# Optimization experiments

Measured on AMD Instinct MI355X. Metric: run time of the kernel, lower is better.

The kernel has to match this reference:

```python
import jax, jax.numpy as jnp
import numpy as np

B_, S, D = 4, 1024, 1024
MULT, HEAD_DIM, M, K, CFAC = 4, 64, 16, 2, 1.25
H = MULT * D


def _layer_norm(x, g, b, eps=1e-5):
    mu = jnp.mean(x, axis=-1, keepdims=True)
    var = jnp.var(x, axis=-1, keepdims=True)
    return (x - mu) * jax.lax.rsqrt(var + eps) * g + b


def setup_inputs() -> dict:
    key = jax.random.key(0)
    ks = jax.random.split(key, 10)
    sc = 0.02
    return {
        "x": jax.random.normal(ks[0], (B_, S, D), jnp.float32),
        "ln1_g": jnp.ones((D,), jnp.float32), "ln1_b": jnp.zeros((D,), jnp.float32),
        "qkv_w": jax.random.normal(ks[1], (3 * D, D), jnp.float32) * sc,
        "qkv_b": jnp.zeros((3 * D,), jnp.float32),
        "attn_in_w": jax.random.normal(ks[2], (3 * D, D), jnp.float32) * sc,
        "attn_in_b": jnp.zeros((3 * D,), jnp.float32),
        "attn_out_w": jax.random.normal(ks[3], (D, D), jnp.float32) * sc,
        "attn_out_b": jnp.zeros((D,), jnp.float32),
        "ln2_g": jnp.ones((D,), jnp.float32), "ln2_b": jnp.zeros((D,), jnp.float32),
        "r_w1": jax.random.normal(ks[4], (H, D), jnp.float32) * sc,
        "r_b1": jnp.zeros((H,), jnp.float32),
        "r_w2": jax.random.normal(ks[5], (M, H), jnp.float32) * sc,
        "r_b2": jnp.zeros((M,), jnp.float32),
        "mlp1": jax.random.normal(ks[6], (M, D, H), jnp.float32) / np.float32(np.sqrt(D)),
        "mlp2": jax.random.normal(ks[7], (M, H, D), jnp.float32) / np.float32(np.sqrt(H)),
    }


def reference(x, ln1_g, ln1_b, qkv_w, qkv_b, attn_in_w, attn_in_b,
              attn_out_w, attn_out_b, ln2_g, ln2_b, r_w1, r_b1, r_w2, r_b2,
              mlp1, mlp2):
    b, s, d = x.shape
    nh, hd = d // HEAD_DIM, HEAD_DIM

    # ---- attention block ----
    resid = x
    xn = _layer_norm(x, ln1_g, ln1_b)
    qkv = xn @ qkv_w.T + qkv_b              # [b,s,3d]
    q0, k0, v0 = jnp.split(qkv, 3, axis=-1)
    # nn.MultiheadAttention applies its own in/out projections on top
    wq, wk, wv = jnp.split(attn_in_w, 3, axis=0)
    bq, bk, bv = jnp.split(attn_in_b, 3, axis=0)
    q = (q0 @ wq.T + bq).reshape(b, s, nh, hd).transpose(0, 2, 1, 3)
    k = (k0 @ wk.T + bk).reshape(b, s, nh, hd).transpose(0, 2, 1, 3)
    v = (v0 @ wv.T + bv).reshape(b, s, nh, hd).transpose(0, 2, 1, 3)
    scores = jnp.einsum('bhqd,bhkd->bhqk', q, k) / np.float32(np.sqrt(hd))
    causal = jnp.triu(jnp.full((s, s), -jnp.inf, jnp.float32), k=1)
    attn = jax.nn.softmax(scores + causal, axis=-1)
    ao = jnp.einsum('bhqk,bhkd->bhqd', attn, v).transpose(0, 2, 1, 3).reshape(b, s, d)
    x1 = resid + (ao @ attn_out_w.T + attn_out_b)

    # ---- MoE MLP block ----
    resid2 = x1
    xn2 = _layer_norm(x1, ln2_g, ln2_b)
    B = b * s
    cap = int(B * CFAC * K // M)
    xf = xn2.reshape(B, d)
    # router
    logits = jax.nn.gelu(xf @ r_w1.T + r_b1, approximate=False) @ r_w2.T + r_b2  # [B,M]
    vals, inds = jax.lax.top_k(logits, K)
    probs = jax.nn.softmax(vals, axis=-1).reshape(-1)     # [B*K]
    indsf = inds.reshape(-1)                              # [B*K]
    # cumsum-based position within each expert's capacity buffer
    one_hot = jax.nn.one_hot(indsf, M, dtype=jnp.int32)
    counts = jnp.cumsum(one_hot, axis=0)
    pos = counts[jnp.arange(B * K), indsf] - 1
    keep = pos < cap
    flat_idx = indsf * cap + pos
    safe_idx = jnp.where(keep, flat_idx, M * cap)         # OOB index -> dropped
    src = jnp.repeat(xf, K, axis=0)                       # [B*K, d]
    expert_in = jnp.zeros((M * cap, d), xf.dtype).at[safe_idx].set(src, mode='drop')
    expert_in = expert_in.reshape(M, cap, d)
    # grouped GEMM experts
    mid = jax.nn.gelu(jnp.einsum('mcd,mdh->mch', expert_in, mlp1), approximate=False)
    eout = jnp.einsum('mch,mhd->mcd', mid, mlp2).reshape(M * cap, d)
    # combine
    g = eout[jnp.where(keep, flat_idx, 0)] * (probs * keep)[:, None]
    token_idx = jnp.repeat(jnp.arange(B), K)
    combined = jax.ops.segment_sum(g, token_idx, num_segments=B)
    has_kept = jax.ops.segment_sum(keep.astype(jnp.int32), token_idx, num_segments=B) > 0
    moe_out = jnp.where(has_kept[:, None], combined, xf)
    out = resid2 + moe_out.reshape(b, s, d)
    return out, logits.reshape(b, s, M)
```

## Files before the change

kernel.cpp:

```cpp
#include <hip/hip_runtime.h>
#include <math.h>

#define NTOK   4096
#define DIM    1024
#define H3     3072
#define HMLP   4096
#define NEXP   16
#define CAP    640
#define HCHUNK 1024
#define LSCALE 2048.0f
#define INV_LSCALE (1.0f / 2048.0f)

typedef _Float16 half8 __attribute__((ext_vector_type(8)));
typedef __attribute__((ext_vector_type(4))) float floatx4;
typedef __attribute__((ext_vector_type(8))) ushort us8;

#define F_QKV_HI   ((size_t)0)
#define F_QKV_LO   ((size_t)6291456)
#define F_XN_HI    ((size_t)12582912)
#define F_XN_LO    ((size_t)14680064)
#define F_H1       ((size_t)0)
#define F_EOUT     ((size_t)0)
#define F_Q16_HI   ((size_t)16777216)
#define F_K16_HI   ((size_t)18874368)
#define F_V16_HI   ((size_t)20971520)
#define F_Q16_LO   ((size_t)23068672)
#define F_K16_LO   ((size_t)25165824)
#define F_V16_LO   ((size_t)27262976)
#define F_VT_HI    ((size_t)12582912)
#define F_VT_LO    ((size_t)14680064)
#define F_AO_HI    ((size_t)29360128)
#define F_AO_LO    ((size_t)31457280)
#define F_XF_HI    ((size_t)33554432)
#define F_XF_LO    ((size_t)35651584)
#define F_WQKV_HI  ((size_t)37748736)
#define F_WQKV_LO  ((size_t)39321600)
#define F_WAIN_HI  ((size_t)40894464)
#define F_WAIN_LO  ((size_t)42467328)
#define F_WAOUT_HI ((size_t)44040192)
#define F_WAOUT_LO ((size_t)44564480)
#define F_WR1_HI   ((size_t)45088768)
#define F_WR1_LO   ((size_t)47185920)
#define F_EXPIN    ((size_t)16777216)
#define F_MLP1T    ((size_t)22020096)
#define F_MID      ((size_t)30408704)
#define F_MLP2T    ((size_t)35651584)
#define F_X1       ((size_t)49283072)
#define F_XF       ((size_t)53477376)
#define F_PROBS    ((size_t)57671680)
#define F_INDS     ((size_t)57679872)
#define F_KEEP     ((size_t)57688064)
#define F_FLAT     ((size_t)57696256)

__device__ __forceinline__ ushort f2h(float f) {
    _Float16 h = (_Float16)f;
    union { _Float16 h; ushort u; } c; c.h = h; return c.u;
}
__device__ __forceinline__ float h2f(ushort u) {
    union { ushort u; _Float16 h; } c; c.u = u; return (float)c.h;
}
__device__ __forceinline__ float gelu_exact(float x) {
    return 0.5f * x * (1.0f + erff(x * 0.7071067811865475f));
}

__global__ __launch_bounds__(256) void split_f32(const float* __restrict__ x,
                                                 ushort* __restrict__ hi,
                                                 ushort* __restrict__ lo, int n4) {
    int i = blockIdx.x * 256 + threadIdx.x;
    if (i >= n4) return;
    float4 v = ((const float4*)x)[i];
    float vv[4] = {v.x, v.y, v.z, v.w};
    ushort h[4], l[4];
#pragma unroll
    for (int e = 0; e < 4; e++) {
        h[e] = f2h(vv[e]);
        l[e] = f2h((vv[e] - h2f(h[e])) * LSCALE);
    }
    ((ushort4*)hi)[i] = make_ushort4(h[0], h[1], h[2], h[3]);
    ((ushort4*)lo)[i] = make_ushort4(l[0], l[1], l[2], l[3]);
}

__global__ __launch_bounds__(256) void ln_kernel(const float* __restrict__ x,
                                                 const float* __restrict__ g,
                                                 const float* __restrict__ b,
                                                 float* __restrict__ yf,
                                                 ushort* __restrict__ yhi,
                                                 ushort* __restrict__ ylo) {
    __shared__ float red0[4], red1[4], bc[2];
    const size_t t = blockIdx.x;
    const float* row = x + t * DIM;
    float v[4];
    float s = 0.f, s2 = 0.f;
#pragma unroll
    for (int i = 0; i < 4; i++) {
        float vv = row[threadIdx.x + i * 256];
        v[i] = vv; s += vv; s2 += vv * vv;
    }
#pragma unroll
    for (int off = 32; off > 0; off >>= 1) {
        s  += __shfl_down(s, off);
        s2 += __shfl_down(s2, off);
    }
    const int lane = threadIdx.x & 63, wid = threadIdx.x >> 6;
    if (lane == 0) { red0[wid] = s; red1[wid] = s2; }
    __syncthreads();
    if (threadIdx.x == 0) {
        float S = red0[0] + red0[1] + red0[2] + red0[3];
        float S2 = red1[0] + red1[1] + red1[2] + red1[3];
        float mean = S * (1.0f / DIM);
        float var = S2 * (1.0f / DIM) - mean * mean;
        bc[0] = mean; bc[1] = rsqrtf(var + 1e-5f);
    }
    __syncthreads();
    const float mean = bc[0], r = bc[1];
#pragma unroll
    for (int i = 0; i < 4; i++) {
        int idx = threadIdx.x + i * 256;
        float val = (v[i] - mean) * r * g[idx] + b[idx];
        size_t o = t * DIM + idx;
        if (yf) yf[o] = val;
        if (yhi) {
            ushort h = f2h(val);
            yhi[o] = h;
            if (ylo) ylo[o] = f2h((val - h2f(h)) * LSCALE);
        }
    }
}

template<bool SPLIT>
__global__ __launch_bounds__(256) void gemm_ht(
    const ushort* __restrict__ Ahi, const ushort* __restrict__ Alo, int lda, long long sA,
    const ushort* __restrict__ Bhi, const ushort* __restrict__ Blo, int ldb, long long sB,
    const float* __restrict__ bias, long long sBias,
    const float* __restrict__ resid, int ldr,
    float* __restrict__ outf, ushort* __restrict__ outhi, ushort* __restrict__ outlo,
    int ldc, long long sC, int Kdim, int act, int accum) {
    __shared__ ushort sAh[128][40];
    __shared__ ushort sBh[128][40];
    __shared__ ushort sAl[SPLIT ? 128 : 1][40];
    __shared__ ushort sBl[SPLIT ? 128 : 1][40];
    const int z = blockIdx.z;
    Ahi += (size_t)z * sA; Bhi += (size_t)z * sB;
    if constexpr (SPLIT) { Alo += (size_t)z * sA; Blo += (size_t)z * sB; }
    if (bias) bias += (size_t)z * sBias;
    if (outf) outf += (size_t)z * sC;
    if (outhi) outhi += (size_t)z * sC;
    if (outlo) outlo += (size_t)z * sC;

    const int tid = threadIdx.x;
    const int row0 = blockIdx.y * 128, col0 = blockIdx.x * 128;
    const int sr = tid >> 2, skq = (tid & 3) * 8;
    const int lane = tid & 63;
    const int m = lane & 15, half = lane >> 4;
    const int w = tid >> 6;
    const int ar0 = (w >> 1) * 64, bc0 = (w & 1) * 64;

    floatx4 acc[4][4];
    floatx4 acc2[SPLIT ? 4 : 1][SPLIT ? 4 : 1];
#pragma unroll
    for (int i = 0; i < 4; i++)
#pragma unroll
        for (int j = 0; j < 4; j++) acc[i][j] = (floatx4){0.f, 0.f, 0.f, 0.f};
    if constexpr (SPLIT) {
#pragma unroll
        for (int i = 0; i < 4; i++)
#pragma unroll
            for (int j = 0; j < 4; j++) acc2[i][j] = (floatx4){0.f, 0.f, 0.f, 0.f};
    }

    for (int k0 = 0; k0 < Kdim; k0 += 32) {
        uint4 a0 = *(const uint4*)(Ahi + (size_t)(row0 + sr) * lda + k0 + skq);
        uint4 a1 = *(const uint4*)(Ahi + (size_t)(row0 + sr + 64) * lda + k0 + skq);
        uint4 b0 = *(const uint4*)(Bhi + (size_t)(col0 + sr) * ldb + k0 + skq);
        uint4 b1 = *(const uint4*)(Bhi + (size_t)(col0 + sr + 64) * ldb + k0 + skq);
        uint4 a2, a3, b2, b3;
        if constexpr (SPLIT) {
            a2 = *(const uint4*)(Alo + (size_t)(row0 + sr) * lda + k0 + skq);
            a3 = *(const uint4*)(Alo + (size_t)(row0 + sr + 64) * lda + k0 + skq);
            b2 = *(const uint4*)(Blo + (size_t)(col0 + sr) * ldb + k0 + skq);
            b3 = *(const uint4*)(Blo + (size_t)(col0 + sr + 64) * ldb + k0 + skq);
        }
        __syncthreads();
        *(uint4*)&sAh[sr][skq] = a0;
        *(uint4*)&sAh[sr + 64][skq] = a1;
        *(uint4*)&sBh[sr][skq] = b0;
        *(uint4*)&sBh[sr + 64][skq] = b1;
        if constexpr (SPLIT) {
            *(uint4*)&sAl[sr][skq] = a2;
            *(uint4*)&sAl[sr + 64][skq] = a3;
            *(uint4*)&sBl[sr][skq] = b2;
            *(uint4*)&sBl[sr + 64][skq] = b3;
        }
        __syncthreads();
        half8 fa[4], fb[4], fal[4], fbl[4];
#pragma unroll
        for (int i = 0; i < 4; i++) fa[i] = *(const half8*)&sAh[ar0 + i * 16 + m][half * 8];
#pragma unroll
        for (int j = 0; j < 4; j++) fb[j] = *(const half8*)&sBh[bc0 + j * 16 + m][half * 8];
        if constexpr (SPLIT) {
#pragma unroll
            for (int i = 0; i < 4; i++) fal[i] = *(const half8*)&sAl[ar0 + i * 16 + m][half * 8];
#pragma unroll
            for (int j = 0; j < 4; j++) fbl[j] = *(const half8*)&sBl[bc0 + j * 16 + m][half * 8];
        }
#pragma unroll
        for (int i = 0; i < 4; i++)
#pragma unroll
            for (int j = 0; j < 4; j++) {
                acc[i][j] = __builtin_amdgcn_mfma_f32_16x16x32_f16(fa[i], fb[j], acc[i][j], 0, 0, 0);
                if constexpr (SPLIT) {
                    acc2[i][j] = __builtin_amdgcn_mfma_f32_16x16x32_f16(fa[i], fbl[j], acc2[i][j], 0, 0, 0);
                    acc2[i][j] = __builtin_amdgcn_mfma_f32_16x16x32_f16(fal[i], fb[j], acc2[i][j], 0, 0, 0);
                }
            }
    }
#pragma unroll
    for (int i = 0; i < 4; i++) {
#pragma unroll
        for (int j = 0; j < 4; j++) {
            const int col = col0 + bc0 + j * 16 + m;
            const float bv = bias ? bias[col] : 0.f;
#pragma unroll
            for (int r = 0; r < 4; r++) {
                const int row = row0 + ar0 + i * 16 + half * 4 + r;
                float v = acc[i][j][r];
                if constexpr (SPLIT) v += acc2[i][j][r] * INV_LSCALE;
                v += bv;
                if (resid) v += resid[(size_t)row * ldr + col];
                if (accum) v += outf[(size_t)row * ldc + col];
                if (act) v = gelu_exact(v);
                const size_t o = (size_t)row * ldc + col;
                if (outf) outf[o] = v;
                if (outhi) {
                    ushort h = f2h(v);
                    outhi[o] = h;
                    if (outlo) outlo[o] = f2h((v - h2f(h)) * LSCALE);
                }
            }
        }
    }
}

__global__ __launch_bounds__(256) void transpose_h(const float* __restrict__ in, long long sIn, int ldin,
                                                   ushort* __restrict__ out, long long sOut, int ldout) {
    __shared__ float t[32][33];
    const int z = blockIdx.z;
    in += (size_t)z * sIn; out += (size_t)z * sOut;
    const int cx = threadIdx.x & 31, ry = threadIdx.x >> 5;
    const int r0 = blockIdx.y * 32, c0 = blockIdx.x * 32;
#pragma unroll
    for (int rr = 0; rr < 4; rr++)
        t[ry + rr * 8][cx] = in[(size_t)(r0 + ry + rr * 8) * ldin + c0 + cx];
    __syncthreads();
#pragma unroll
    for (int rr = 0; rr < 4; rr++)
        out[(size_t)(c0 + ry + rr * 8) * ldout + r0 + cx] = f2h(t[cx][ry + rr * 8]);
}

__global__ __launch_bounds__(256) void vtrans_kernel(const ushort* __restrict__ vhi,
                                                     const ushort* __restrict__ vlo,
                                                     ushort* __restrict__ vthi,
                                                     ushort* __restrict__ vtlo) {
    __shared__ ushort th[32][72], tl[32][72];
    const int bh = blockIdx.y, b = bh >> 4, h = bh & 15;
    const int s0 = blockIdx.x * 32;
    const int t = threadIdx.x;
    {
        const int s = t >> 3, d0 = (t & 7) * 8;
        const size_t src = ((size_t)(b * 1024 + s0 + s)) * 1024 + h * 64 + d0;
        *(uint4*)&th[s][d0] = *(const uint4*)&vhi[src];
        *(uint4*)&tl[s][d0] = *(const uint4*)&vlo[src];
    }
    __syncthreads();
    {
        const int d = t >> 2, soff = (t & 3) * 8;
        us8 rh, rl;
#pragma unroll
        for (int e = 0; e < 8; e++) { rh[e] = th[soff + e][d]; rl[e] = tl[soff + e][d]; }
        const size_t dst = (size_t)bh * 65536 + (size_t)d * 1024 + s0 + soff;
        *(us8*)&vthi[dst] = rh;
        *(us8*)&vtlo[dst] = rl;
    }
}

__global__ __launch_bounds__(256, 2) void attn_mfma(
        const ushort* __restrict__ qh_, const ushort* __restrict__ ql_,
        const ushort* __restrict__ kh_, const ushort* __restrict__ kl_,
        const ushort* __restrict__ vth_, const ushort* __restrict__ vtl_,
        ushort* __restrict__ ao_hi, ushort* __restrict__ ao_lo) {
    __shared__ ushort plds[4][2][2048];
    const int bh = blockIdx.y;
    const int b = bh >> 4;
    const int qt = 7 - blockIdx.x;
    const int tid = threadIdx.x;
    const int w = tid >> 6, lane = tid & 63;
    const int m = lane & 15, hq = lane >> 4;
    const int wrow = qt * 128 + w * 32;
    const size_t cbase = ((size_t)b * 1024) * 1024 + (size_t)(bh & 15) * 64;
    const size_t vtbase = (size_t)bh * 65536;

    half8 qfh[2][2], qfl[2][2];
#pragma unroll
    for (int i = 0; i < 2; i++)
#pragma unroll
        for (int kk = 0; kk < 2; kk++) {
            const size_t o = cbase + (size_t)(wrow + i * 16 + m) * 1024 + kk * 32 + hq * 8;
            qfh[i][kk] = *(const half8*)&qh_[o];
            qfl[i][kk] = *(const half8*)&ql_[o];
        }

    floatx4 accO[2][4], accO2[2][4];
#pragma unroll
    for (int i = 0; i < 2; i++)
#pragma unroll
        for (int d = 0; d < 4; d++) {
            accO[i][d] = (floatx4){0.f, 0.f, 0.f, 0.f};
            accO2[i][d] = (floatx4){0.f, 0.f, 0.f, 0.f};
        }
    float mx[2][4], ls[2][4];
#pragma unroll
    for (int i = 0; i < 2; i++)
#pragma unroll
        for (int r = 0; r < 4; r++) { mx[i][r] = -3.0e38f; ls[i][r] = 0.f; }

    const int ntiles = (wrow + 31) / 64 + 1;
    for (int t = 0; t < ntiles; t++) {
        const int j0 = t * 64;
        floatx4 accS[2][4], accS2[2][4];
#pragma unroll
        for (int i = 0; i < 2; i++)
#pragma unroll
            for (int jf = 0; jf < 4; jf++) {
                accS[i][jf] = (floatx4){0.f, 0.f, 0.f, 0.f};
                accS2[i][jf] = (floatx4){0.f, 0.f, 0.f, 0.f};
            }
#pragma unroll
        for (int kk = 0; kk < 2; kk++) {
            half8 kfh[4], kfl[4];
#pragma unroll
            for (int jf = 0; jf < 4; jf++) {
                const size_t o = cbase + (size_t)(j0 + jf * 16 + m) * 1024 + kk * 32 + hq * 8;
                kfh[jf] = *(const half8*)&kh_[o];
                kfl[jf] = *(const half8*)&kl_[o];
            }
#pragma unroll
            for (int i = 0; i < 2; i++)
#pragma unroll
                for (int jf = 0; jf < 4; jf++) {
                    accS[i][jf] = __builtin_amdgcn_mfma_f32_16x16x32_f16(qfh[i][kk], kfh[jf], accS[i][jf], 0, 0, 0);
                    accS2[i][jf] = __builtin_amdgcn_mfma_f32_16x16x32_f16(qfh[i][kk], kfl[jf], accS2[i][jf], 0, 0, 0);
                    accS2[i][jf] = __builtin_amdgcn_mfma_f32_16x16x32_f16(qfl[i][kk], kfh[jf], accS2[i][jf], 0, 0, 0);
                }
        }
        const bool diag = (j0 + 63 > wrow);
        float p[2][4][4];
#pragma unroll
        for (int i = 0; i < 2; i++)
#pragma unroll
            for (int jf = 0; jf < 4; jf++)
#pragma unroll
                for (int r = 0; r < 4; r++) {
                    float s = (accS[i][jf][r] + accS2[i][jf][r] * INV_LSCALE) * 0.125f;
                    if (diag && (j0 + jf * 16 + m > wrow + i * 16 + hq * 4 + r)) s = -3.0e38f;
                    p[i][jf][r] = s;
                }
#pragma unroll
        for (int i = 0; i < 2; i++)
#pragma unroll
            for (int r = 0; r < 4; r++) {
                float tm = fmaxf(fmaxf(p[i][0][r], p[i][1][r]), fmaxf(p[i][2][r], p[i][3][r]));
#pragma unroll
                for (int off = 8; off > 0; off >>= 1) tm = fmaxf(tm, __shfl_xor(tm, off));
                const float mn = fmaxf(mx[i][r], tm);
                const float c = __expf(mx[i][r] - mn);
                mx[i][r] = mn;
                float rs = 0.f;
#pragma unroll
                for (int jf = 0; jf < 4; jf++) {
                    const float e = __expf(p[i][jf][r] - mn);
                    p[i][jf][r] = e;
                    rs += e;
                }
#pragma unroll
                for (int off = 8; off > 0; off >>= 1) rs += __shfl_xor(rs, off);
                ls[i][r] = ls[i][r] * c + rs;
#pragma unroll
                for (int d = 0; d < 4; d++) { accO[i][d][r] *= c; accO2[i][d][r] *= c; }
            }
#pragma unroll
        for (int i = 0; i < 2; i++)
#pragma unroll
            for (int jf = 0; jf < 4; jf++)
#pragma unroll
                for (int r = 0; r < 4; r++) {
                    const int row = i * 16 + hq * 4 + r;
                    const int idx = row * 64 + ((jf * 16 + m) ^ ((row & 7) << 3));
                    const float pv = p[i][jf][r];
                    const ushort hh = f2h(pv);
                    plds[w][0][idx] = hh;
                    plds[w][1][idx] = f2h((pv - h2f(hh)) * LSCALE);
                }
#pragma unroll
        for (int kk = 0; kk < 2; kk++) {
            half8 pfh[2], pfl[2], vfh[4], vfl[4];
#pragma unroll
            for (int i = 0; i < 2; i++) {
                const int row = i * 16 + m;
                const int idx = row * 64 + ((kk * 32 + hq * 8) ^ ((row & 7) << 3));
                pfh[i] = *(const half8*)&plds[w][0][idx];
                pfl[i] = *(const half8*)&plds[w][1][idx];
            }
#pragma unroll
            for (int d = 0; d < 4; d++) {
                const size_t o = vtbase + (size_t)(d * 16 + m) * 1024 + j0 + kk * 32 + hq * 8;
                vfh[d] = *(const half8*)&vth_[o];
                vfl[d] = *(const half8*)&vtl_[o];
            }
#pragma unroll
            for (int i = 0; i < 2; i++)
#pragma unroll
                for (int d = 0; d < 4; d++) {
                    accO[i][d] = __builtin_amdgcn_mfma_f32_16x16x32_f16(pfh[i], vfh[d], accO[i][d], 0, 0, 0);
                    accO2[i][d] = __builtin_amdgcn_mfma_f32_16x16x32_f16(pfh[i], vfl[d], accO2[i][d], 0, 0, 0);
                    accO2[i][d] = __builtin_amdgcn_mfma_f32_16x16x32_f16(pfl[i], vfh[d], accO2[i][d], 0, 0, 0);
                }
        }
    }
#pragma unroll
    for (int i = 0; i < 2; i++)
#pragma unroll
        for (int r = 0; r < 4; r++) {
            const float inv = 1.f / ls[i][r];
            const size_t rb = cbase + (size_t)(wrow + i * 16 + hq * 4 + r) * 1024;
#pragma unroll
            for (int d = 0; d < 4; d++) {
                const float v = (accO[i][d][r] + accO2[i][d][r] * INV_LSCALE) * inv;
                const ushort hh = f2h(v);
                const size_t o = rb + d * 16 + m;
                ao_hi[o] = hh;
                ao_lo[o] = f2h((v - h2f(hh)) * LSCALE);
            }
        }
}

__global__ __launch_bounds__(256) void router2_kernel(const float* __restrict__ h1,
                                                      const float* __restrict__ w2,
                                                      const float* __restrict__ b2,
                                                      float* __restrict__ logits_out,
                                                      float* __restrict__ probs,
                                                      int* __restrict__ inds) {
    __shared__ float red[16][4];
    __shared__ float lg[16];
    const int t = blockIdx.x;
    const float* hrow = h1 + (size_t)t * HMLP;
    float acc[16];
#pragma unroll
    for (int m = 0; m < 16; m++) acc[m] = 0.f;
    for (int i = 0; i < 16; i++) {
        int kk = threadIdx.x + i * 256;
        float hv = hrow[kk];
#pragma unroll
        for (int m = 0; m < 16; m++) acc[m] = fmaf(hv, w2[m * HMLP + kk], acc[m]);
    }
#pragma unroll
    for (int m = 0; m < 16; m++)
#pragma unroll
        for (int off = 32; off > 0; off >>= 1) acc[m] += __shfl_down(acc[m], off);
    const int lane = threadIdx.x & 63, wid = threadIdx.x >> 6;
    if (lane == 0) {
#pragma unroll
        for (int m = 0; m < 16; m++) red[m][wid] = acc[m];
    }
    __syncthreads();
    if (threadIdx.x < 16) {
        float v = red[threadIdx.x][0] + red[threadIdx.x][1] + red[threadIdx.x][2] + red[threadIdx.x][3]
                  + b2[threadIdx.x];
        lg[threadIdx.x] = v;
        logits_out[(size_t)t * 16 + threadIdx.x] = v;
    }
    __syncthreads();
    if (threadIdx.x == 0) {
        int i0 = 0; float v0 = lg[0];
        for (int m = 1; m < 16; m++) if (lg[m] > v0) { v0 = lg[m]; i0 = m; }
        int i1 = -1; float v1 = -3.4e38f;
        for (int m = 0; m < 16; m++) if (m != i0 && lg[m] > v1) { v1 = lg[m]; i1 = m; }
        float e1 = expf(v1 - v0);
        float den = 1.f + e1;
        inds[2 * t] = i0; inds[2 * t + 1] = i1;
        probs[2 * t] = 1.f / den; probs[2 * t + 1] = e1 / den;
    }
}

__global__ __launch_bounds__(256) void scan_kernel(const int* __restrict__ inds,
                                                   int* __restrict__ keep,
                                                   int* __restrict__ flat) {
    __shared__ int counts[256][16];
    const int t = threadIdx.x;
#pragma unroll
    for (int e = 0; e < 16; e++) counts[t][e] = 0;
    const int base = t * 32;
    for (int i = 0; i < 32; i++) counts[t][inds[base + i]]++;
    __syncthreads();
    if (t < 16) {
        int run = 0;
        for (int c = 0; c < 256; c++) { int tmp = counts[c][t]; counts[c][t] = run; run += tmp; }
    }
    __syncthreads();
    for (int i = 0; i < 32; i++) {
        int e = inds[base + i];
        int p = counts[t][e]++;
        keep[base + i] = (p < CAP) ? 1 : 0;
        flat[base + i] = e * CAP + p;
    }
}

__global__ __launch_bounds__(256) void scatter_kernel(const float* __restrict__ xf,
                                                      const int* __restrict__ keep,
                                                      const int* __restrict__ flat,
                                                      ushort* __restrict__ expert_in) {
    const int e = blockIdx.x;
    if (!keep[e]) return;
    const int token = e >> 1;
    const float* src = xf + (size_t)token * DIM;
    ushort* dst = expert_in + (size_t)flat[e] * DIM;
#pragma unroll
    for (int i = 0; i < 4; i++) dst[threadIdx.x + i * 256] = f2h(src[threadIdx.x + i * 256]);
}

__global__ __launch_bounds__(256) void combine_kernel(const float* __restrict__ x1,
                                                      const float* __restrict__ xf,
                                                      const float* __restrict__ eout,
                                                      const float* __restrict__ probs,
                                                      const int* __restrict__ keep,
                                                      const int* __restrict__ flat,
                                                      float* __restrict__ out) {
    const int t = blockIdx.x;
    const int k0 = keep[2 * t], k1 = keep[2 * t + 1];
    const float p0 = probs[2 * t], p1 = probs[2 * t + 1];
    const size_t f0 = (size_t)flat[2 * t] * DIM, f1 = (size_t)flat[2 * t + 1] * DIM;
    const bool has = (k0 || k1);
    const size_t base = (size_t)t * DIM;
#pragma unroll
    for (int i = 0; i < 4; i++) {
        const int idx = threadIdx.x + i * 256;
        float mo;
        if (has) {
            mo = 0.f;
            if (k0) mo += p0 * eout[f0 + idx];
            if (k1) mo += p1 * eout[f1 + idx];
        } else {
            mo = xf[base + idx];
        }
        out[base + idx] = x1[base + idx] + mo;
    }
}

extern "C" void kernel_launch(void* const* d_in, const int* in_sizes, int n_in,
                              void* d_out, int out_size, void* d_ws, size_t ws_size,
                              hipStream_t stream) {
    const float* x          = (const float*)d_in[0];
    const float* ln1_g      = (const float*)d_in[1];
    const float* ln1_b      = (const float*)d_in[2];
    const float* qkv_w      = (const float*)d_in[3];
    const float* qkv_b      = (const float*)d_in[4];
    const float* attn_in_w  = (const float*)d_in[5];
    const float* attn_in_b  = (const float*)d_in[6];
    const float* attn_out_w = (const float*)d_in[7];
    const float* attn_out_b = (const float*)d_in[8];
    const float* ln2_g      = (const float*)d_in[9];
    const float* ln2_b      = (const float*)d_in[10];
    const float* r_w1       = (const float*)d_in[11];
    const float* r_b1       = (const float*)d_in[12];
    const float* r_w2       = (const float*)d_in[13];
    const float* r_b2       = (const float*)d_in[14];
    const float* mlp1       = (const float*)d_in[15];
    const float* mlp2       = (const float*)d_in[16];

    float* ws = (float*)d_ws;
    ushort* qkv_hi   = (ushort*)(ws + F_QKV_HI);
    ushort* qkv_lo   = (ushort*)(ws + F_QKV_LO);
    ushort* xn_hi    = (ushort*)(ws + F_XN_HI);
    ushort* xn_lo    = (ushort*)(ws + F_XN_LO);
    float*  h1       = ws + F_H1;
    float*  eout     = ws + F_EOUT;
    ushort* q_hi     = (ushort*)(ws + F_Q16_HI);
    ushort* q_lo     = (ushort*)(ws + F_Q16_LO);
    ushort* v_hi     = (ushort*)(ws + F_V16_HI);
    ushort* v_lo     = (ushort*)(ws + F_V16_LO);
    ushort* k_hi     = (ushort*)(ws + F_K16_HI);
    ushort* k_lo     = (ushort*)(ws + F_K16_LO);
    ushort* vt_hi    = (ushort*)(ws + F_VT_HI);
    ushort* vt_lo    = (ushort*)(ws + F_VT_LO);
    ushort* ao_hi    = (ushort*)(ws + F_AO_HI);
    ushort* ao_lo    = (ushort*)(ws + F_AO_LO);
    ushort* xf_hi    = (ushort*)(ws + F_XF_HI);
    ushort* xf_lo    = (ushort*)(ws + F_XF_LO);
    ushort* wqkv_hi  = (ushort*)(ws + F_WQKV_HI);
    ushort* wqkv_lo  = (ushort*)(ws + F_WQKV_LO);
    ushort* wain_hi  = (ushort*)(ws + F_WAIN_HI);
    ushort* wain_lo  = (ushort*)(ws + F_WAIN_LO);
    ushort* waout_hi = (ushort*)(ws + F_WAOUT_HI);
    ushort* waout_lo = (ushort*)(ws + F_WAOUT_LO);
    ushort* wr1_hi   = (ushort*)(ws + F_WR1_HI);
    ushort* wr1_lo   = (ushort*)(ws + F_WR1_LO);
    ushort* expert_in= (ushort*)(ws + F_EXPIN);
    ushort* mlp1t    = (ushort*)(ws + F_MLP1T);
    ushort* mid      = (ushort*)(ws + F_MID);
    ushort* mlp2t    = (ushort*)(ws + F_MLP2T);
    float*  x1       = ws + F_X1;
    float*  xf       = ws + F_XF;
    float*  probs    = ws + F_PROBS;
    int*    inds     = (int*)(ws + F_INDS);
    int*    keep     = (int*)(ws + F_KEEP);
    int*    flat     = (int*)(ws + F_FLAT);

    float* out        = (float*)d_out;
    float* logits_out = out + (size_t)NTOK * DIM;

    split_f32<<<(3145728 / 4 + 255) / 256, 256, 0, stream>>>(qkv_w, wqkv_hi, wqkv_lo, 3145728 / 4);
    split_f32<<<(3145728 / 4 + 255) / 256, 256, 0, stream>>>(attn_in_w, wain_hi, wain_lo, 3145728 / 4);
    split_f32<<<(1048576 / 4 + 255) / 256, 256, 0, stream>>>(attn_out_w, waout_hi, waout_lo, 1048576 / 4);
    split_f32<<<(4194304 / 4 + 255) / 256, 256, 0, stream>>>(r_w1, wr1_hi, wr1_lo, 4194304 / 4);

    ln_kernel<<<NTOK, 256, 0, stream>>>(x, ln1_g, ln1_b, nullptr, xn_hi, xn_lo);
    gemm_ht<true><<<dim3(H3 / 128, NTOK / 128, 1), 256, 0, stream>>>(
        xn_hi, xn_lo, DIM, 0, wqkv_hi, wqkv_lo, DIM, 0, qkv_b, 0,
        nullptr, 0, nullptr, qkv_hi, qkv_lo, H3, 0, DIM, 0, 0);
    gemm_ht<true><<<dim3(DIM / 128, NTOK / 128, 3), 256, 0, stream>>>(
        qkv_hi, qkv_lo, H3, 1024, wain_hi, wain_lo, DIM, 1048576, attn_in_b, 1024,
        nullptr, 0, nullptr, q_hi, q_lo, DIM, 4194304, DIM, 0, 0);
    vtrans_kernel<<<dim3(32, 64), 256, 0, stream>>>(v_hi, v_lo, vt_hi, vt_lo);
    attn_mfma<<<dim3(8, 64), 256, 0, stream>>>(q_hi, q_lo, k_hi, k_lo, vt_hi, vt_lo, ao_hi, ao_lo);
    gemm_ht<true><<<dim3(DIM / 128, NTOK / 128, 1), 256, 0, stream>>>(
        ao_hi, ao_lo, DIM, 0, waout_hi, waout_lo, DIM, 0, attn_out_b, 0,
        x, DIM, x1, nullptr, nullptr, DIM, 0, DIM, 0, 0);
    ln_kernel<<<NTOK, 256, 0, stream>>>(x1, ln2_g, ln2_b, xf, xf_hi, xf_lo);
    gemm_ht<true><<<dim3(HMLP / 128, NTOK / 128, 1), 256, 0, stream>>>(
        xf_hi, xf_lo, DIM, 0, wr1_hi, wr1_lo, DIM, 0, r_b1, 0,
        nullptr, 0, h1, nullptr, nullptr, HMLP, 0, DIM, 1, 0);
    router2_kernel<<<NTOK, 256, 0, stream>>>(h1, r_w2, r_b2, logits_out, probs, inds);
    scan_kernel<<<1, 256, 0, stream>>>(inds, keep, flat);
    scatter_kernel<<<NTOK * 2, 256, 0, stream>>>(xf, keep, flat, expert_in);
    for (int c = 0; c < HMLP / HCHUNK; c++) {
        transpose_h<<<dim3(32, 32, NEXP), 256, 0, stream>>>(
            mlp1 + (size_t)c * HCHUNK, (long long)DIM * HMLP, HMLP, mlp1t, 1048576, DIM);
        gemm_ht<false><<<dim3(HCHUNK / 128, CAP / 128, NEXP), 256, 0, stream>>>(
            expert_in, nullptr, DIM, 655360, mlp1t, nullptr, DIM, 1048576, nullptr, 0,
            nullptr, 0, nullptr, mid, nullptr, HCHUNK, 655360, DIM, 1, 0);
        transpose_h<<<dim3(32, 32, NEXP), 256, 0, stream>>>(
            mlp2 + (size_t)c * HCHUNK * DIM, (long long)HMLP * DIM, DIM, mlp2t, 1048576, HCHUNK);
        gemm_ht<false><<<dim3(DIM / 128, CAP / 128, NEXP), 256, 0, stream>>>(
            mid, nullptr, HCHUNK, 655360, mlp2t, nullptr, HCHUNK, 1048576, nullptr, 0,
            nullptr, 0, eout, nullptr, nullptr, DIM, 655360, HCHUNK, 0, c > 0);
    }
    combine_kernel<<<NTOK, 256, 0, stream>>>(x1, xf, eout, probs, keep, flat, out);
}
```

Baseline: 2.315 ms.

## Load GEMM tiles directly into LDS with global_load_lds and XOR swizzle

Replaces the register-staged global→LDS tile copies in the half-precision GEMM with direct global_load_lds 16-byte transfers. The padded LDS rows (40) become unpadded (32), and an XOR swizzle on both the write column and the fragment read column is meant to avoid bank conflicts. This cuts VGPR use and copy instructions, but the loads are still issued right after a barrier with no double buffering, so the latency is not hidden. It also depends on the swizzle mapping matching between writer and reader.

```diff
diff --git a/kernel.cpp b/kernel.cpp
--- a/kernel.cpp
+++ b/kernel.cpp
@@ -63,6 +63,12 @@
     return 0.5f * x * (1.0f + erff(x * 0.7071067811865475f));
 }
 
+__device__ __forceinline__ void gl16(const void* g, void* l) {
+    __builtin_amdgcn_global_load_lds(
+        (const __attribute__((address_space(1))) void*)g,
+        (__attribute__((address_space(3))) void*)l, 16, 0, 0);
+}
+
 __global__ __launch_bounds__(256) void split_f32(const float* __restrict__ x,
                                                  ushort* __restrict__ hi,
                                                  ushort* __restrict__ lo, int n4) {
@@ -135,10 +141,10 @@
     const float* __restrict__ resid, int ldr,
     float* __restrict__ outf, ushort* __restrict__ outhi, ushort* __restrict__ outlo,
     int ldc, long long sC, int Kdim, int act, int accum) {
-    __shared__ ushort sAh[128][40];
-    __shared__ ushort sBh[128][40];
-    __shared__ ushort sAl[SPLIT ? 128 : 1][40];
-    __shared__ ushort sBl[SPLIT ? 128 : 1][40];
+    __shared__ ushort sAh[128][32];
+    __shared__ ushort sBh[128][32];
+    __shared__ ushort sAl[SPLIT ? 128 : 1][32];
+    __shared__ ushort sBl[SPLIT ? 128 : 1][32];
     const int z = blockIdx.z;
     Ahi += (size_t)z * sA; Bhi += (size_t)z * sB;
     if constexpr (SPLIT) { Alo += (size_t)z * sA; Blo += (size_t)z * sB; }
@@ -149,12 +155,15 @@
 
     const int tid = threadIdx.x;
     const int row0 = blockIdx.y * 128, col0 = blockIdx.x * 128;
-    const int sr = tid >> 2, skq = (tid & 3) * 8;
     const int lane = tid & 63;
     const int m = lane & 15, half = lane >> 4;
     const int w = tid >> 6;
     const int ar0 = (w >> 1) * 64, bc0 = (w & 1) * 64;
 
+    const int srow = w * 32 + (lane >> 2);
+    const int ssw  = (((lane >> 3) & 3) ^ (lane & 3)) * 8;
+    const int rsw8 = ((((m >> 1) & 3) ^ half)) * 8;
+
     floatx4 acc[4][4];
     floatx4 acc2[SPLIT ? 4 : 1][SPLIT ? 4 : 1];
 #pragma unroll
@@ -169,39 +178,34 @@
     }
 
     for (int k0 = 0; k0 < Kdim; k0 += 32) {
-        uint4 a0 = *(const uint4*)(Ahi + (size_t)(row0 + sr) * lda + k0 + skq);
-        uint4 a1 = *(const uint4*)(Ahi + (size_t)(row0 + sr + 64) * lda + k0 + skq);
-        uint4 b0 = *(const uint4*)(Bhi + (size_t)(col0 + sr) * ldb + k0 + skq);
-        uint4 b1 = *(const uint4*)(Bhi + (size_t)(col0 + sr + 64) * ldb + k0 + skq);
-        uint4 a2, a3, b2, b3;
-        if constexpr (SPLIT) {
-            a2 = *(const uint4*)(Alo + (size_t)(row0 + sr) * lda + k0 + skq);
-            a3 = *(const uint4*)(Alo + (size_t)(row0 + sr + 64) * lda + k0 + skq);
-            b2 = *(const uint4*)(Blo + (size_t)(col0 + sr) * ldb + k0 + skq);
-            b3 = *(const uint4*)(Blo + (size_t)(col0 + sr + 64) * ldb + k0 + skq);
-        }
         __syncthreads();
-        *(uint4*)&sAh[sr][skq] = a0;
-        *(uint4*)&sAh[sr + 64][skq] = a1;
-        *(uint4*)&sBh[sr][skq] = b0;
-        *(uint4*)&sBh[sr + 64][skq] = b1;
-        if constexpr (SPLIT) {
-            *(uint4*)&sAl[sr][skq] = a2;
-            *(uint4*)&sAl[sr + 64][skq] = a3;
-            *(uint4*)&sBl[sr][skq] = b2;
-            *(uint4*)&sBl[sr + 64][skq] = b3;
+        {
+            const ushort* gA = Ahi + (size_t)(row0 + srow) * lda + k0 + ssw;
+            const ushort* gB = Bhi + (size_t)(col0 + srow) * ldb + k0 + ssw;
+            gl16(gA,                      &sAh[w * 32][0]);
+            gl16(gA + (size_t)16 * lda,   &sAh[w * 32 + 16][0]);
+            gl16(gB,                      &sBh[w * 32][0]);
+            gl16(gB + (size_t)16 * ldb,   &sBh[w * 32 + 16][0]);
+            if constexpr (SPLIT) {
+                const ushort* gAl = Alo + (size_t)(row0 + srow) * lda + k0 + ssw;
+                const ushort* gBl = Blo + (size_t)(col0 + srow) * ldb + k0 + ssw;
+                gl16(gAl,                    &sAl[w * 32][0]);
+                gl16(gAl + (size_t)16 * lda, &sAl[w * 32 + 16][0]);
+                gl16(gBl,                    &sBl[w * 32][0]);
+                gl16(gBl + (size_t)16 * ldb, &sBl[w * 32 + 16][0]);
+            }
         }
         __syncthreads();
         half8 fa[4], fb[4], fal[4], fbl[4];
 #pragma unroll
-        for (int i = 0; i < 4; i++) fa[i] = *(const half8*)&sAh[ar0 + i * 16 + m][half * 8];
-#pragma unroll
-        for (int j = 0; j < 4; j++) fb[j] = *(const half8*)&sBh[bc0 + j * 16 + m][half * 8];
+        for (int i = 0; i < 4; i++) fa[i] = *(const half8*)&sAh[ar0 + i * 16 + m][rsw8];
+#pragma unroll
+        for (int j = 0; j < 4; j++) fb[j] = *(const half8*)&sBh[bc0 + j * 16 + m][rsw8];
         if constexpr (SPLIT) {
 #pragma unroll
-            for (int i = 0; i < 4; i++) fal[i] = *(const half8*)&sAl[ar0 + i * 16 + m][half * 8];
-#pragma unroll
-            for (int j = 0; j < 4; j++) fbl[j] = *(const half8*)&sBl[bc0 + j * 16 + m][half * 8];
+            for (int i = 0; i < 4; i++) fal[i] = *(const half8*)&sAl[ar0 + i * 16 + m][rsw8];
+#pragma unroll
+            for (int j = 0; j < 4; j++) fbl[j] = *(const half8*)&sBl[bc0 + j * 16 + m][rsw8];
         }
 #pragma unroll
         for (int i = 0; i < 4; i++)
```

New measurement: 2.283 ms. No clear change (-1.4%).
